# Kernel tuning notes

Measured on AMD Instinct MI355X. Metric: run time of the kernel, lower is better.

The kernel has to match this reference:

```python
import jax, jax.numpy as jnp
import numpy as np

B, L, D, H, R = 2, 128, 256, 8, 4
DK = D // H  # 32
EPS = 1e-6


def setup_inputs() -> dict:
    key = jax.random.key(0)
    ks = jax.random.split(key, 12)
    q = jax.random.normal(ks[0], (B, L, D), jnp.float32)
    k = jax.random.normal(ks[1], (B, L, D), jnp.float32)
    v = jax.random.normal(ks[2], (B, L, D), jnp.float32)
    t = jnp.sort(jax.random.uniform(ks[3], (B, L), jnp.float32), axis=-1)
    omega = jax.random.uniform(ks[4], (B, L, L), jnp.float32)
    mask = jnp.triu(jnp.ones((L, L), bool), 1)  # True = masked (causal)
    xav = (2.0 / (D + D)) ** 0.5
    Wq = jax.random.normal(ks[5], (D, H * DK), jnp.float32) * xav
    Wk = jax.random.normal(ks[6], (D, H * DK), jnp.float32) * xav
    Wv = jax.random.normal(ks[7], (D, H * DK), jnp.float32) * xav
    s = jax.random.uniform(ks[8], (R,), jnp.float32) + 0.1  # ODE time-decay scales
    fc_w = jax.random.normal(ks[9], (H * DK, D), jnp.float32) * xav
    fc_b = jnp.zeros((D,), jnp.float32)
    ln_g = jnp.ones((D,), jnp.float32)
    ln_b = jnp.zeros((D,), jnp.float32)
    return {"q": q, "k": k, "v": v, "t": t, "omega": omega, "mask": mask,
            "Wq": Wq, "Wk": Wk, "Wv": Wv, "s": s,
            "fc_w": fc_w, "fc_b": fc_b, "ln_g": ln_g, "ln_b": ln_b}


def _ode_proj(x, W, phi):
    # x: (B,L,D), W: (D,H*DK), phi: (B,L,L,R) time kernel
    p = x @ W                                       # (B,L,H*DK)
    y = p[:, None, :, None, :] * phi[..., None]     # (B,L,L,R,H*DK)
    y = y.reshape(B, L, L, R, H, DK)
    return y.transpose(0, 4, 1, 2, 3, 5)            # (B,H,L,L,R,DK)


def reference(q, k, v, t, omega, mask, Wq, Wk, Wv, s, fc_w, fc_b, ln_g, ln_b):
    temp = DK ** 0.5
    residual = q
    # pre-LayerNorm on q (normalize_before=True)
    mu = q.mean(-1, keepdims=True)
    var = q.var(-1, keepdims=True)
    qn = (q - mu) / jnp.sqrt(var + EPS) * ln_g + ln_b
    # continuous-time kernel phi[b,i,j,r] = exp(-|t_i - t_j| * s_r)
    dt = jnp.abs(t[:, :, None] - t[:, None, :])     # (B,L,L)
    phi = jnp.exp(-dt[..., None] * s)               # (B,L,L,R)
    q6 = _ode_proj(qn, Wq, phi)                     # (B,H,L,L,R,DK)
    k6 = _ode_proj(k, Wk, phi)
    v6 = _ode_proj(v, Wv, phi)
    # attn = (q/temp * k * omega).sum(-1).sum(-1)
    attn = jnp.einsum('bhijrd,bhijrd,bij->bhij', q6 / temp, k6, omega)
    attn = jnp.where(mask[None, None, :, :], -1e9, attn)
    attn = jax.nn.softmax(attn, axis=-1)            # (B,H,L,L)
    vsum = v6.sum(axis=4)                           # sum over R -> (B,H,L,L,DK)
    out = jnp.einsum('bhij,bhijd->bhid', attn, vsum)  # (B,H,L,DK)
    out = out.transpose(0, 2, 1, 3).reshape(B, L, H * DK)
    out = out @ fc_w + fc_b + residual              # dropout = identity (eval)
    return (out, attn)
```

## Files before the change

kernel.cpp:

```cpp
#include <hip/hip_runtime.h>

#define B_  2
#define L_  128
#define D_  256
#define H_  8
#define R_  4
#define DK_ 32
#define BL_ (B_*L_)
#define SXP 260
#define SQH 132
#define SWP 129

__device__ __forceinline__ float wredsum64(float v) {
    #pragma unroll
    for (int m = 32; m >= 1; m >>= 1) v += __shfl_xor(v, m, 64);
    return v;
}
__device__ __forceinline__ float wredmax64(float v) {
    #pragma unroll
    for (int m = 32; m >= 1; m >>= 1) v = fmaxf(v, __shfl_xor(v, m, 64));
    return v;
}

__global__ __launch_bounds__(256) void k_proj(
    const float* __restrict__ q, const float* __restrict__ k, const float* __restrict__ v,
    const float* __restrict__ Wq, const float* __restrict__ Wk, const float* __restrict__ Wv,
    const float* __restrict__ ln_g, const float* __restrict__ ln_b,
    float* __restrict__ pv, float* __restrict__ qkpart)
{
    const int blk = blockIdx.x;
    const int rowTile = blk >> 4;
    const int cg = blk & 15;
    const int rbase = rowTile * 4;
    const int tid = threadIdx.x;

    __shared__ __align__(16) float sx[3][4 * SXP];
    __shared__ __align__(16) float partF[16 * 4 * 16];
    __shared__ float spq[4][16], spk[4][16];

    {
        const int r = tid >> 6, f4c = tid & 63;
        #pragma unroll
        for (int p = 0; p < 3; ++p) {
            const float* src = (p == 0 ? q : (p == 1 ? k : v)) + (size_t)(rbase + r) * D_;
            *reinterpret_cast<float4*>(&sx[p][r * SXP + f4c * 4]) =
                reinterpret_cast<const float4*>(src)[f4c];
        }
    }
    __syncthreads();

    {
        const int r = tid >> 6, lane = tid & 63;
        float x0 = sx[0][r * SXP + lane];
        float x1 = sx[0][r * SXP + lane + 64];
        float x2 = sx[0][r * SXP + lane + 128];
        float x3 = sx[0][r * SXP + lane + 192];
        float s1 = x0 + x1 + x2 + x3;
        float s2 = x0*x0 + x1*x1 + x2*x2 + x3*x3;
        #pragma unroll
        for (int m = 32; m >= 1; m >>= 1) {
            s1 += __shfl_xor(s1, m, 64);
            s2 += __shfl_xor(s2, m, 64);
        }
        const float mu = s1 * (1.0f / D_);
        const float rs = rsqrtf(s2 * (1.0f / D_) - mu * mu + 1e-6f);
        sx[0][r * SXP + lane      ] = (x0 - mu) * rs * ln_g[lane      ] + ln_b[lane      ];
        sx[0][r * SXP + lane +  64] = (x1 - mu) * rs * ln_g[lane +  64] + ln_b[lane +  64];
        sx[0][r * SXP + lane + 128] = (x2 - mu) * rs * ln_g[lane + 128] + ln_b[lane + 128];
        sx[0][r * SXP + lane + 192] = (x3 - mu) * rs * ln_g[lane + 192] + ln_b[lane + 192];
    }
    __syncthreads();

    const int kg  = tid >> 4;
    const int row = (tid >> 2) & 3;
    const int c4  = tid & 3;
    const int gc4 = cg * 4 + c4;
    const int kbase = kg * 16;

    #pragma unroll
    for (int m = 0; m < 3; ++m) {
        const float4* W4 = reinterpret_cast<const float4*>(m == 0 ? Wq : (m == 1 ? Wk : Wv));
        float4 a = {0, 0, 0, 0};
        #pragma unroll
        for (int kk = 0; kk < 16; ++kk) {
            const int kr = kbase + kk;
            const float x = sx[m][row * SXP + kr];
            const float4 w = W4[kr * 64 + gc4];
            a.x += x * w.x; a.y += x * w.y; a.z += x * w.z; a.w += x * w.w;
        }
        *reinterpret_cast<float4*>(&partF[(kg * 16 + row * 4 + c4) * 4]) = a;
        __syncthreads();
        if (tid < 64) {
            const int rr = tid >> 4, cc = tid & 15;
            float sum = 0.f;
            #pragma unroll
            for (int g = 0; g < 16; ++g) sum += partF[g * 64 + rr * 16 + cc];
            if      (m == 0) spq[rr][cc] = sum;
            else if (m == 1) spk[rr][cc] = sum;
            else             pv[(size_t)(rbase + rr) * D_ + cg * 16 + cc] = sum;
        }
        __syncthreads();
    }

    if (tid < 64) {
        const int rr = tid >> 4, cc = tid & 15;
        float d = spq[rr][cc] * spk[rr][cc];
        #pragma unroll
        for (int m = 8; m >= 1; m >>= 1) d += __shfl_xor(d, m, 64);
        if (cc == 0) qkpart[(size_t)(rbase + rr) * 16 + cg] = d;
    }
}

__global__ __launch_bounds__(512) void k_attn(
    const float* __restrict__ t, const float* __restrict__ omega, const float* __restrict__ s,
    const float* __restrict__ pv, const float* __restrict__ qkpart,
    const float* __restrict__ fc_w, const float* __restrict__ fc_b,
    const float* __restrict__ q, float* __restrict__ dout)
{
    const int blk   = blockIdx.x;
    const int b     = blk >> 5;
    const int itile = blk & 31;
    const int ibase = itile * 4;
    const int tid = threadIdx.x;
    const int w = tid >> 6, lane = tid & 63;

    __shared__ __align__(16) float sQKp[L_ * 16];
    __shared__ __align__(16) float sQKh[H_ * SQH];
    __shared__ __align__(16) float sOm[4 * L_];
    __shared__ __align__(16) float sPhi[4 * L_], sPsi[4 * L_];
    __shared__ __align__(16) float sW[H_ * 4 * SWP];
    __shared__ __align__(16) float partF[8 * 4 * 64 * 4];
    __shared__ __align__(16) float sMid[4 * SXP];
    __shared__ float st[L_], sS[R_];

    {
        const float4* qkp4 = reinterpret_cast<const float4*>(qkpart + (size_t)b * L_ * 16);
        reinterpret_cast<float4*>(sQKp)[tid] = qkp4[tid];
        if (tid < 128)
            reinterpret_cast<float4*>(sOm)[tid] =
                reinterpret_cast<const float4*>(omega + ((size_t)(b * L_ + ibase)) * L_)[tid];
        if (tid < 32)
            reinterpret_cast<float4*>(st)[tid] =
                reinterpret_cast<const float4*>(t + (size_t)b * L_)[tid];
        if (tid < R_) sS[tid] = s[tid];
    }
    __syncthreads();

    {
        const int wi = tid >> 7, j = tid & 127;
        const float dtv = fabsf(st[ibase + wi] - st[j]);
        float Phi = 0.f, Psi = 0.f;
        #pragma unroll
        for (int r = 0; r < R_; ++r) {
            const float e = expf(-dtv * sS[r]);
            Phi += e;
            Psi += e * e;
        }
        sPhi[wi * L_ + j] = Phi;
        sPsi[wi * L_ + j] = Psi;
    }
    #pragma unroll
    for (int p = 0; p < 2; ++p) {
        const int idx = tid + p * 512;
        const int j = idx >> 3, h = idx & 7;
        sQKh[h * SQH + j] = sQKp[j * 16 + 2 * h] + sQKp[j * 16 + 2 * h + 1];
    }
    __syncthreads();

    {
        const int il = w >> 1;
        const int i  = ibase + il;
        const int hb = (w & 1) * 4;
        const float invtemp = 0.17677669529663687f;
        const int j0 = lane, j1 = lane + 64;
        const float c0 = sOm[il*L_ + j0] * sPsi[il*L_ + j0] * invtemp;
        const float c1 = sOm[il*L_ + j1] * sPsi[il*L_ + j1] * invtemp;
        const float ph0 = sPhi[il*L_ + j0], ph1 = sPhi[il*L_ + j1];
        #pragma unroll
        for (int hh = 0; hh < 4; ++hh) {
            const int h = hb + hh;
            float l0 = (j0 <= i) ? c0 * sQKh[h * SQH + j0] : -3.0e38f;
            float l1 = (j1 <= i) ? c1 * sQKh[h * SQH + j1] : -3.0e38f;
            const float mx = wredmax64(fmaxf(l0, l1));
            const float e0 = (j0 <= i) ? expf(l0 - mx) : 0.f;
            const float e1 = (j1 <= i) ? expf(l1 - mx) : 0.f;
            const float inv = 1.0f / wredsum64(e0 + e1);
            const float a0 = e0 * inv, a1 = e1 * inv;
            const size_t ab = (size_t)BL_ * D_ + (((size_t)(b * H_ + h) * L_ + i) * L_);
            dout[ab + j0] = a0;
            dout[ab + j1] = a1;
            sW[(h * 4 + il) * SWP + j0] = a0 * ph0;
            sW[(h * 4 + il) * SWP + j1] = a1 * ph1;
        }
    }
    __syncthreads();

    {
        const int c = lane, jg = w;
        const int h = c >> 3;
        const float4* pv4 = reinterpret_cast<const float4*>(pv + (size_t)b * L_ * D_);
        float4 acc[4];
        #pragma unroll
        for (int il = 0; il < 4; ++il) acc[il] = make_float4(0, 0, 0, 0);
        #pragma unroll
        for (int jj = 0; jj < 16; ++jj) {
            const int j = jg * 16 + jj;
            const float4 p = pv4[j * 64 + c];
            #pragma unroll
            for (int il = 0; il < 4; ++il) {
                const float wgt = sW[(h * 4 + il) * SWP + j];
                acc[il].x += wgt * p.x; acc[il].y += wgt * p.y;
                acc[il].z += wgt * p.z; acc[il].w += wgt * p.w;
            }
        }
        #pragma unroll
        for (int il = 0; il < 4; ++il)
            *reinterpret_cast<float4*>(&partF[((jg * 4 + il) * 64 + c) * 4]) = acc[il];
    }
    __syncthreads();
    if (tid < 256) {
        const int il = tid >> 6, c = tid & 63;
        float4 sum = make_float4(0, 0, 0, 0);
        #pragma unroll
        for (int g = 0; g < 8; ++g) {
            const float4 p = *reinterpret_cast<float4*>(&partF[((g * 4 + il) * 64 + c) * 4]);
            sum.x += p.x; sum.y += p.y; sum.z += p.z; sum.w += p.w;
        }
        *reinterpret_cast<float4*>(&sMid[il * SXP + c * 4]) = sum;
    }
    __syncthreads();

    {
        const int kseg = w, c4 = lane;
        const float4* fw4 = reinterpret_cast<const float4*>(fc_w);
        float4 acc[4];
        #pragma unroll
        for (int r = 0; r < 4; ++r) acc[r] = make_float4(0, 0, 0, 0);
        #pragma unroll
        for (int kk = 0; kk < 32; ++kk) {
            const int k = kseg * 32 + kk;
            const float4 wv = fw4[k * 64 + c4];
            #pragma unroll
            for (int r = 0; r < 4; ++r) {
                const float x = sMid[r * SXP + k];
                acc[r].x += x * wv.x; acc[r].y += x * wv.y;
                acc[r].z += x * wv.z; acc[r].w += x * wv.w;
            }
        }
        #pragma unroll
        for (int r = 0; r < 4; ++r)
            *reinterpret_cast<float4*>(&partF[((kseg * 4 + r) * 64 + c4) * 4]) = acc[r];
    }
    __syncthreads();
    if (tid < 256) {
        const int r = tid >> 6, c4 = tid & 63;
        const float4 bb = reinterpret_cast<const float4*>(fc_b)[c4];
        const float4 res = reinterpret_cast<const float4*>(q)[((size_t)(b * L_ + ibase + r)) * 64 + c4];
        float4 sum = make_float4(bb.x + res.x, bb.y + res.y, bb.z + res.z, bb.w + res.w);
        #pragma unroll
        for (int g = 0; g < 8; ++g) {
            const float4 p = *reinterpret_cast<float4*>(&partF[((g * 4 + r) * 64 + c4) * 4]);
            sum.x += p.x; sum.y += p.y; sum.z += p.z; sum.w += p.w;
        }
        reinterpret_cast<float4*>(dout)[((size_t)(b * L_ + ibase + r)) * 64 + c4] = sum;
    }
}

extern "C" void kernel_launch(void* const* d_in, const int* in_sizes, int n_in,
                              void* d_out, int out_size, void* d_ws, size_t ws_size,
                              hipStream_t stream) {
    const float* q     = (const float*)d_in[0];
    const float* k     = (const float*)d_in[1];
    const float* v     = (const float*)d_in[2];
    const float* t     = (const float*)d_in[3];
    const float* omega = (const float*)d_in[4];
    const float* Wq    = (const float*)d_in[6];
    const float* Wk    = (const float*)d_in[7];
    const float* Wv    = (const float*)d_in[8];
    const float* s     = (const float*)d_in[9];
    const float* fc_w  = (const float*)d_in[10];
    const float* fc_b  = (const float*)d_in[11];
    const float* ln_g  = (const float*)d_in[12];
    const float* ln_b  = (const float*)d_in[13];

    float* ws     = (float*)d_ws;
    float* pv     = ws;
    float* qkpart = ws + 65536;
    float* out    = (float*)d_out;

    hipLaunchKernelGGL(k_proj, dim3(1024), dim3(256), 0, stream,
                       q, k, v, Wq, Wk, Wv, ln_g, ln_b, pv, qkpart);
    hipLaunchKernelGGL(k_attn, dim3(64), dim3(512), 0, stream,
                       t, omega, s, pv, qkpart, fc_w, fc_b, q, out);
}
```

Baseline: 96.67 us.

## Fuse projection and attention into one cooperative kernel with grid sync

Merges the projection kernel and the attention kernel into a single cooperative launch of 256 blocks of 512 threads, separated by a grid-wide barrier, with shared memory reused through a union. The projection stage is retiled so each block computes 64 output columns for 4 rows and does the Q, K and V products in one fused loop. The goal is to remove the second launch and the inter-kernel gap. In exchange it adds grid-sync overhead, leaves most blocks idle after the barrier, and each block now holds the larger shared-memory footprint.

```diff
diff --git a/kernel.cpp b/kernel.cpp
--- a/kernel.cpp
+++ b/kernel.cpp
@@ -1,4 +1,5 @@
 #include <hip/hip_runtime.h>
+#include <hip/hip_cooperative_groups.h>
 
 #define B_  2
 #define L_  128
@@ -11,6 +12,8 @@
 #define SQH 132
 #define SWP 129
 
+namespace cg = cooperative_groups;
+
 __device__ __forceinline__ float wredsum64(float v) {
     #pragma unroll
     for (int m = 32; m >= 1; m >>= 1) v += __shfl_xor(v, m, 64);
@@ -22,148 +25,159 @@
     return v;
 }
 
-__global__ __launch_bounds__(256) void k_proj(
+struct __align__(16) SMemA {
+    float sx[3][4 * SXP];
+    float partF[3][2048];
+};
+struct __align__(16) SMemB {
+    float sQKp[2048];
+    float sQKh[H_ * SQH];
+    float sOm[4 * L_];
+    float sPhi[4 * L_];
+    float sPsi[4 * L_];
+    float sW[H_ * 4 * SWP];
+    float partF[8192];
+    float sMid[4 * SXP];
+    float st[L_];
+    float sS[R_];
+};
+union __align__(16) SMem { SMemA a; SMemB b; };
+
+__global__ __launch_bounds__(512) void k_fused(
     const float* __restrict__ q, const float* __restrict__ k, const float* __restrict__ v,
     const float* __restrict__ Wq, const float* __restrict__ Wk, const float* __restrict__ Wv,
     const float* __restrict__ ln_g, const float* __restrict__ ln_b,
-    float* __restrict__ pv, float* __restrict__ qkpart)
+    const float* __restrict__ t, const float* __restrict__ omega, const float* __restrict__ s,
+    const float* __restrict__ fc_w, const float* __restrict__ fc_b,
+    float* __restrict__ pv, float* __restrict__ qkpart, float* __restrict__ dout)
 {
+    __shared__ SMem sm;
     const int blk = blockIdx.x;
-    const int rowTile = blk >> 4;
-    const int cg = blk & 15;
-    const int rbase = rowTile * 4;
     const int tid = threadIdx.x;
 
-    __shared__ __align__(16) float sx[3][4 * SXP];
-    __shared__ __align__(16) float partF[16 * 4 * 16];
-    __shared__ float spq[4][16], spk[4][16];
-
-    {
-        const int r = tid >> 6, f4c = tid & 63;
-        #pragma unroll
-        for (int p = 0; p < 3; ++p) {
+    {
+        const int rowTile = blk >> 2;
+        const int cgA     = blk & 3;
+        const int rbase   = rowTile * 4;
+
+        for (int i = tid; i < 768; i += 512) {
+            const int p = i >> 8, r = (i >> 6) & 3, f4c = i & 63;
             const float* src = (p == 0 ? q : (p == 1 ? k : v)) + (size_t)(rbase + r) * D_;
-            *reinterpret_cast<float4*>(&sx[p][r * SXP + f4c * 4]) =
+            *reinterpret_cast<float4*>(&sm.a.sx[p][r * SXP + f4c * 4]) =
                 reinterpret_cast<const float4*>(src)[f4c];
         }
-    }
-    __syncthreads();
-
-    {
-        const int r = tid >> 6, lane = tid & 63;
-        float x0 = sx[0][r * SXP + lane];
-        float x1 = sx[0][r * SXP + lane + 64];
-        float x2 = sx[0][r * SXP + lane + 128];
-        float x3 = sx[0][r * SXP + lane + 192];
-        float s1 = x0 + x1 + x2 + x3;
-        float s2 = x0*x0 + x1*x1 + x2*x2 + x3*x3;
-        #pragma unroll
-        for (int m = 32; m >= 1; m >>= 1) {
-            s1 += __shfl_xor(s1, m, 64);
-            s2 += __shfl_xor(s2, m, 64);
-        }
-        const float mu = s1 * (1.0f / D_);
-        const float rs = rsqrtf(s2 * (1.0f / D_) - mu * mu + 1e-6f);
-        sx[0][r * SXP + lane      ] = (x0 - mu) * rs * ln_g[lane      ] + ln_b[lane      ];
-        sx[0][r * SXP + lane +  64] = (x1 - mu) * rs * ln_g[lane +  64] + ln_b[lane +  64];
-        sx[0][r * SXP + lane + 128] = (x2 - mu) * rs * ln_g[lane + 128] + ln_b[lane + 128];
-        sx[0][r * SXP + lane + 192] = (x3 - mu) * rs * ln_g[lane + 192] + ln_b[lane + 192];
-    }
-    __syncthreads();
-
-    const int kg  = tid >> 4;
-    const int row = (tid >> 2) & 3;
-    const int c4  = tid & 3;
-    const int gc4 = cg * 4 + c4;
-    const int kbase = kg * 16;
-
-    #pragma unroll
-    for (int m = 0; m < 3; ++m) {
-        const float4* W4 = reinterpret_cast<const float4*>(m == 0 ? Wq : (m == 1 ? Wk : Wv));
-        float4 a = {0, 0, 0, 0};
-        #pragma unroll
-        for (int kk = 0; kk < 16; ++kk) {
+        __syncthreads();
+
+        if (tid < 256) {
+            const int r = tid >> 6, lane = tid & 63;
+            float x0 = sm.a.sx[0][r * SXP + lane];
+            float x1 = sm.a.sx[0][r * SXP + lane + 64];
+            float x2 = sm.a.sx[0][r * SXP + lane + 128];
+            float x3 = sm.a.sx[0][r * SXP + lane + 192];
+            float s1 = x0 + x1 + x2 + x3;
+            float s2 = x0*x0 + x1*x1 + x2*x2 + x3*x3;
+            #pragma unroll
+            for (int m = 32; m >= 1; m >>= 1) {
+                s1 += __shfl_xor(s1, m, 64);
+                s2 += __shfl_xor(s2, m, 64);
+            }
+            const float mu = s1 * (1.0f / D_);
+            const float rs = rsqrtf(s2 * (1.0f / D_) - mu * mu + 1e-6f);
+            sm.a.sx[0][r * SXP + lane      ] = (x0 - mu) * rs * ln_g[lane      ] + ln_b[lane      ];
+            sm.a.sx[0][r * SXP + lane +  64] = (x1 - mu) * rs * ln_g[lane +  64] + ln_b[lane +  64];
+            sm.a.sx[0][r * SXP + lane + 128] = (x2 - mu) * rs * ln_g[lane + 128] + ln_b[lane + 128];
+            sm.a.sx[0][r * SXP + lane + 192] = (x3 - mu) * rs * ln_g[lane + 192] + ln_b[lane + 192];
+        }
+        __syncthreads();
+
+        const int kg  = tid >> 6;
+        const int row = (tid >> 4) & 3;
+        const int c4  = tid & 15;
+        const int gc4 = cgA * 16 + c4;
+        const int kbase = kg * 32;
+        const float4* Wq4 = reinterpret_cast<const float4*>(Wq);
+        const float4* Wk4 = reinterpret_cast<const float4*>(Wk);
+        const float4* Wv4 = reinterpret_cast<const float4*>(Wv);
+        float4 aq = {0,0,0,0}, ak = {0,0,0,0}, av = {0,0,0,0};
+        #pragma unroll 8
+        for (int kk = 0; kk < 32; ++kk) {
             const int kr = kbase + kk;
-            const float x = sx[m][row * SXP + kr];
-            const float4 w = W4[kr * 64 + gc4];
-            a.x += x * w.x; a.y += x * w.y; a.z += x * w.z; a.w += x * w.w;
-        }
-        *reinterpret_cast<float4*>(&partF[(kg * 16 + row * 4 + c4) * 4]) = a;
+            const float xq = sm.a.sx[0][row * SXP + kr];
+            const float xk = sm.a.sx[1][row * SXP + kr];
+            const float xv = sm.a.sx[2][row * SXP + kr];
+            const float4 wq = Wq4[kr * 64 + gc4];
+            const float4 wk = Wk4[kr * 64 + gc4];
+            const float4 wv = Wv4[kr * 64 + gc4];
+            aq.x += xq * wq.x; aq.y += xq * wq.y; aq.z += xq * wq.z; aq.w += xq * wq.w;
+            ak.x += xk * wk.x; ak.y += xk * wk.y; ak.z += xk * wk.z; ak.w += xk * wk.w;
+            av.x += xv * wv.x; av.y += xv * wv.y; av.z += xv * wv.z; av.w += xv * wv.w;
+        }
+        const int pidx = (kg * 64 + row * 16 + c4) * 4;
+        *reinterpret_cast<float4*>(&sm.a.partF[0][pidx]) = aq;
+        *reinterpret_cast<float4*>(&sm.a.partF[1][pidx]) = ak;
+        *reinterpret_cast<float4*>(&sm.a.partF[2][pidx]) = av;
         __syncthreads();
-        if (tid < 64) {
-            const int rr = tid >> 4, cc = tid & 15;
-            float sum = 0.f;
-            #pragma unroll
-            for (int g = 0; g < 16; ++g) sum += partF[g * 64 + rr * 16 + cc];
-            if      (m == 0) spq[rr][cc] = sum;
-            else if (m == 1) spk[rr][cc] = sum;
-            else             pv[(size_t)(rbase + rr) * D_ + cg * 16 + cc] = sum;
-        }
-        __syncthreads();
-    }
-
-    if (tid < 64) {
-        const int rr = tid >> 4, cc = tid & 15;
-        float d = spq[rr][cc] * spk[rr][cc];
-        #pragma unroll
-        for (int m = 8; m >= 1; m >>= 1) d += __shfl_xor(d, m, 64);
-        if (cc == 0) qkpart[(size_t)(rbase + rr) * 16 + cg] = d;
-    }
-}
-
-__global__ __launch_bounds__(512) void k_attn(
-    const float* __restrict__ t, const float* __restrict__ omega, const float* __restrict__ s,
-    const float* __restrict__ pv, const float* __restrict__ qkpart,
-    const float* __restrict__ fc_w, const float* __restrict__ fc_b,
-    const float* __restrict__ q, float* __restrict__ dout)
-{
-    const int blk   = blockIdx.x;
+
+        if (tid < 256) {
+            const int rr = tid >> 6, cf = tid & 63;
+            float sq = 0.f, sk = 0.f, sv = 0.f;
+            #pragma unroll
+            for (int g = 0; g < 8; ++g) {
+                const int idx = g * 256 + rr * 64 + cf;
+                sq += sm.a.partF[0][idx];
+                sk += sm.a.partF[1][idx];
+                sv += sm.a.partF[2][idx];
+            }
+            pv[(size_t)(rbase + rr) * D_ + cgA * 64 + cf] = sv;
+            float d = sq * sk;
+            #pragma unroll
+            for (int m = 8; m >= 1; m >>= 1) d += __shfl_xor(d, m, 64);
+            if ((cf & 15) == 0)
+                qkpart[(size_t)(rbase + rr) * 16 + cgA * 4 + (cf >> 4)] = d;
+        }
+    }
+
+    __threadfence();
+    cg::this_grid().sync();
+
+    if (blk >= 64) return;
+
     const int b     = blk >> 5;
     const int itile = blk & 31;
     const int ibase = itile * 4;
-    const int tid = threadIdx.x;
     const int w = tid >> 6, lane = tid & 63;
 
-    __shared__ __align__(16) float sQKp[L_ * 16];
-    __shared__ __align__(16) float sQKh[H_ * SQH];
-    __shared__ __align__(16) float sOm[4 * L_];
-    __shared__ __align__(16) float sPhi[4 * L_], sPsi[4 * L_];
-    __shared__ __align__(16) float sW[H_ * 4 * SWP];
-    __shared__ __align__(16) float partF[8 * 4 * 64 * 4];
-    __shared__ __align__(16) float sMid[4 * SXP];
-    __shared__ float st[L_], sS[R_];
-
     {
         const float4* qkp4 = reinterpret_cast<const float4*>(qkpart + (size_t)b * L_ * 16);
-        reinterpret_cast<float4*>(sQKp)[tid] = qkp4[tid];
+        reinterpret_cast<float4*>(sm.b.sQKp)[tid] = qkp4[tid];
         if (tid < 128)
-            reinterpret_cast<float4*>(sOm)[tid] =
+            reinterpret_cast<float4*>(sm.b.sOm)[tid] =
                 reinterpret_cast<const float4*>(omega + ((size_t)(b * L_ + ibase)) * L_)[tid];
         if (tid < 32)
-            reinterpret_cast<float4*>(st)[tid] =
+            reinterpret_cast<float4*>(sm.b.st)[tid] =
                 reinterpret_cast<const float4*>(t + (size_t)b * L_)[tid];
-        if (tid < R_) sS[tid] = s[tid];
+        if (tid < R_) sm.b.sS[tid] = s[tid];
     }
     __syncthreads();
 
     {
         const int wi = tid >> 7, j = tid & 127;
-        const float dtv = fabsf(st[ibase + wi] - st[j]);
+        const float dtv = fabsf(sm.b.st[ibase + wi] - sm.b.st[j]);
         float Phi = 0.f, Psi = 0.f;
         #pragma unroll
         for (int r = 0; r < R_; ++r) {
-            const float e = expf(-dtv * sS[r]);
+            const float e = expf(-dtv * sm.b.sS[r]);
             Phi += e;
             Psi += e * e;
         }
-        sPhi[wi * L_ + j] = Phi;
-        sPsi[wi * L_ + j] = Psi;
+        sm.b.sPhi[wi * L_ + j] = Phi;
+        sm.b.sPsi[wi * L_ + j] = Psi;
     }
     #pragma unroll
     for (int p = 0; p < 2; ++p) {
         const int idx = tid + p * 512;
         const int j = idx >> 3, h = idx & 7;
-        sQKh[h * SQH + j] = sQKp[j * 16 + 2 * h] + sQKp[j * 16 + 2 * h + 1];
+        sm.b.sQKh[h * SQH + j] = sm.b.sQKp[j * 16 + 2 * h] + sm.b.sQKp[j * 16 + 2 * h + 1];
     }
     __syncthreads();
 
@@ -173,14 +187,14 @@
         const int hb = (w & 1) * 4;
         const float invtemp = 0.17677669529663687f;
         const int j0 = lane, j1 = lane + 64;
-        const float c0 = sOm[il*L_ + j0] * sPsi[il*L_ + j0] * invtemp;
-        const float c1 = sOm[il*L_ + j1] * sPsi[il*L_ + j1] * invtemp;
-        const float ph0 = sPhi[il*L_ + j0], ph1 = sPhi[il*L_ + j1];
+        const float c0 = sm.b.sOm[il*L_ + j0] * sm.b.sPsi[il*L_ + j0] * invtemp;
+        const float c1 = sm.b.sOm[il*L_ + j1] * sm.b.sPsi[il*L_ + j1] * invtemp;
+        const float ph0 = sm.b.sPhi[il*L_ + j0], ph1 = sm.b.sPhi[il*L_ + j1];
         #pragma unroll
         for (int hh = 0; hh < 4; ++hh) {
             const int h = hb + hh;
-            float l0 = (j0 <= i) ? c0 * sQKh[h * SQH + j0] : -3.0e38f;
-            float l1 = (j1 <= i) ? c1 * sQKh[h * SQH + j1] : -3.0e38f;
+            float l0 = (j0 <= i) ? c0 * sm.b.sQKh[h * SQH + j0] : -3.0e38f;
+            float l1 = (j1 <= i) ? c1 * sm.b.sQKh[h * SQH + j1] : -3.0e38f;
             const float mx = wredmax64(fmaxf(l0, l1));
             const float e0 = (j0 <= i) ? expf(l0 - mx) : 0.f;
             const float e1 = (j1 <= i) ? expf(l1 - mx) : 0.f;
@@ -189,8 +203,8 @@
             const size_t ab = (size_t)BL_ * D_ + (((size_t)(b * H_ + h) * L_ + i) * L_);
             dout[ab + j0] = a0;
             dout[ab + j1] = a1;
-            sW[(h * 4 + il) * SWP + j0] = a0 * ph0;
-            sW[(h * 4 + il) * SWP + j1] = a1 * ph1;
+            sm.b.sW[(h * 4 + il) * SWP + j0] = a0 * ph0;
+            sm.b.sW[(h * 4 + il) * SWP + j1] = a1 * ph1;
         }
     }
     __syncthreads();
@@ -208,14 +222,14 @@
             const float4 p = pv4[j * 64 + c];
             #pragma unroll
             for (int il = 0; il < 4; ++il) {
-                const float wgt = sW[(h * 4 + il) * SWP + j];
+                const float wgt = sm.b.sW[(h * 4 + il) * SWP + j];
                 acc[il].x += wgt * p.x; acc[il].y += wgt * p.y;
                 acc[il].z += wgt * p.z; acc[il].w += wgt * p.w;
             }
         }
         #pragma unroll
         for (int il = 0; il < 4; ++il)
-            *reinterpret_cast<float4*>(&partF[((jg * 4 + il) * 64 + c) * 4]) = acc[il];
+            *reinterpret_cast<float4*>(&sm.b.partF[((jg * 4 + il) * 64 + c) * 4]) = acc[il];
     }
     __syncthreads();
     if (tid < 256) {
@@ -223,10 +237,10 @@
         float4 sum = make_float4(0, 0, 0, 0);
         #pragma unroll
         for (int g = 0; g < 8; ++g) {
-            const float4 p = *reinterpret_cast<float4*>(&partF[((g * 4 + il) * 64 + c) * 4]);
+            const float4 p = *reinterpret_cast<float4*>(&sm.b.partF[((g * 4 + il) * 64 + c) * 4]);
             sum.x += p.x; sum.y += p.y; sum.z += p.z; sum.w += p.w;
         }
-        *reinterpret_cast<float4*>(&sMid[il * SXP + c * 4]) = sum;
+        *reinterpret_cast<float4*>(&sm.b.sMid[il * SXP + c * 4]) = sum;
     }
     __syncthreads();
 
@@ -238,18 +252,18 @@
         for (int r = 0; r < 4; ++r) acc[r] = make_float4(0, 0, 0, 0);
         #pragma unroll
         for (int kk = 0; kk < 32; ++kk) {
-            const int k = kseg * 32 + kk;
-            const float4 wv = fw4[k * 64 + c4];
+            const int kx = kseg * 32 + kk;
+            const float4 wv = fw4[kx * 64 + c4];
             #pragma unroll
             for (int r = 0; r < 4; ++r) {
-                const float x = sMid[r * SXP + k];
+                const float x = sm.b.sMid[r * SXP + kx];
                 acc[r].x += x * wv.x; acc[r].y += x * wv.y;
                 acc[r].z += x * wv.z; acc[r].w += x * wv.w;
             }
         }
         #pragma unroll
         for (int r = 0; r < 4; ++r)
-            *reinterpret_cast<float4*>(&partF[((kseg * 4 + r) * 64 + c4) * 4]) = acc[r];
+            *reinterpret_cast<float4*>(&sm.b.partF[((kseg * 4 + r) * 64 + c4) * 4]) = acc[r];
     }
     __syncthreads();
     if (tid < 256) {
@@ -259,7 +273,7 @@
         float4 sum = make_float4(bb.x + res.x, bb.y + res.y, bb.z + res.z, bb.w + res.w);
         #pragma unroll
         for (int g = 0; g < 8; ++g) {
-            const float4 p = *reinterpret_cast<float4*>(&partF[((g * 4 + r) * 64 + c4) * 4]);
+            const float4 p = *reinterpret_cast<float4*>(&sm.b.partF[((g * 4 + r) * 64 + c4) * 4]);
             sum.x += p.x; sum.y += p.y; sum.z += p.z; sum.w += p.w;
         }
         reinterpret_cast<float4*>(dout)[((size_t)(b * L_ + ibase + r)) * 64 + c4] = sum;
@@ -288,8 +302,13 @@
     float* qkpart = ws + 65536;
     float* out    = (float*)d_out;
 
-    hipLaunchKernelGGL(k_proj, dim3(1024), dim3(256), 0, stream,
-                       q, k, v, Wq, Wk, Wv, ln_g, ln_b, pv, qkpart);
-    hipLaunchKernelGGL(k_attn, dim3(64), dim3(512), 0, stream,
-                       t, omega, s, pv, qkpart, fc_w, fc_b, q, out);
+    void* args[] = {
+        (void*)&q, (void*)&k, (void*)&v,
+        (void*)&Wq, (void*)&Wk, (void*)&Wv,
+        (void*)&ln_g, (void*)&ln_b,
+        (void*)&t, (void*)&omega, (void*)&s,
+        (void*)&fc_w, (void*)&fc_b,
+        (void*)&pv, (void*)&qkpart, (void*)&out
+    };
+    hipLaunchCooperativeKernel((void*)k_fused, dim3(256), dim3(512), args, 0, stream);
 }
```

Measured after the change: 187.3 us. +93.8%, slower.

## Restructure projection to fuse Q/K/V GEMVs and halve attention row tile

Applied to the files above, without the earlier changes.

The projection kernel now computes Q, K and V partial products together in one loop, with 512 threads covering 64 output columns per block. This cuts the block count from 1024 to 256, removes the per-matrix sync and reduce rounds, and makes each block re-read its staged inputs less often. The attention kernel now processes 2 query rows per block instead of 4, doubling the grid to 128 blocks so more compute units are busy. The cost is that fc_w and pv are re-read from global memory by twice as many attention blocks.

```diff
diff --git a/kernel.cpp b/kernel.cpp
--- a/kernel.cpp
+++ b/kernel.cpp
@@ -22,34 +22,30 @@
     return v;
 }
 
-__global__ __launch_bounds__(256) void k_proj(
+__global__ __launch_bounds__(512) void k_proj(
     const float* __restrict__ q, const float* __restrict__ k, const float* __restrict__ v,
     const float* __restrict__ Wq, const float* __restrict__ Wk, const float* __restrict__ Wv,
     const float* __restrict__ ln_g, const float* __restrict__ ln_b,
     float* __restrict__ pv, float* __restrict__ qkpart)
 {
     const int blk = blockIdx.x;
-    const int rowTile = blk >> 4;
-    const int cg = blk & 15;
-    const int rbase = rowTile * 4;
+    const int rowTile = blk >> 2;
+    const int cgA     = blk & 3;
+    const int rbase   = rowTile * 4;
     const int tid = threadIdx.x;
 
     __shared__ __align__(16) float sx[3][4 * SXP];
-    __shared__ __align__(16) float partF[16 * 4 * 16];
-    __shared__ float spq[4][16], spk[4][16];
-
-    {
-        const int r = tid >> 6, f4c = tid & 63;
-        #pragma unroll
-        for (int p = 0; p < 3; ++p) {
-            const float* src = (p == 0 ? q : (p == 1 ? k : v)) + (size_t)(rbase + r) * D_;
-            *reinterpret_cast<float4*>(&sx[p][r * SXP + f4c * 4]) =
-                reinterpret_cast<const float4*>(src)[f4c];
-        }
-    }
-    __syncthreads();
-
-    {
+    __shared__ __align__(16) float partF[3][2048];
+
+    for (int i = tid; i < 768; i += 512) {
+        const int p = i >> 8, r = (i >> 6) & 3, f4c = i & 63;
+        const float* src = (p == 0 ? q : (p == 1 ? k : v)) + (size_t)(rbase + r) * D_;
+        *reinterpret_cast<float4*>(&sx[p][r * SXP + f4c * 4]) =
+            reinterpret_cast<const float4*>(src)[f4c];
+    }
+    __syncthreads();
+
+    if (tid < 256) {
         const int r = tid >> 6, lane = tid & 63;
         float x0 = sx[0][r * SXP + lane];
         float x1 = sx[0][r * SXP + lane + 64];
@@ -71,43 +67,50 @@
     }
     __syncthreads();
 
-    const int kg  = tid >> 4;
-    const int row = (tid >> 2) & 3;
-    const int c4  = tid & 3;
-    const int gc4 = cg * 4 + c4;
-    const int kbase = kg * 16;
-
-    #pragma unroll
-    for (int m = 0; m < 3; ++m) {
-        const float4* W4 = reinterpret_cast<const float4*>(m == 0 ? Wq : (m == 1 ? Wk : Wv));
-        float4 a = {0, 0, 0, 0};
-        #pragma unroll
-        for (int kk = 0; kk < 16; ++kk) {
-            const int kr = kbase + kk;
-            const float x = sx[m][row * SXP + kr];
-            const float4 w = W4[kr * 64 + gc4];
-            a.x += x * w.x; a.y += x * w.y; a.z += x * w.z; a.w += x * w.w;
-        }
-        *reinterpret_cast<float4*>(&partF[(kg * 16 + row * 4 + c4) * 4]) = a;
-        __syncthreads();
-        if (tid < 64) {
-            const int rr = tid >> 4, cc = tid & 15;
-            float sum = 0.f;
-            #pragma unroll
-            for (int g = 0; g < 16; ++g) sum += partF[g * 64 + rr * 16 + cc];
-            if      (m == 0) spq[rr][cc] = sum;
-            else if (m == 1) spk[rr][cc] = sum;
-            else             pv[(size_t)(rbase + rr) * D_ + cg * 16 + cc] = sum;
-        }
-        __syncthreads();
-    }
-
-    if (tid < 64) {
-        const int rr = tid >> 4, cc = tid & 15;
-        float d = spq[rr][cc] * spk[rr][cc];
+    const int kg  = tid >> 6;
+    const int row = (tid >> 4) & 3;
+    const int c4  = tid & 15;
+    const int gc4 = cgA * 16 + c4;
+    const int kbase = kg * 32;
+    const float4* Wq4 = reinterpret_cast<const float4*>(Wq);
+    const float4* Wk4 = reinterpret_cast<const float4*>(Wk);
+    const float4* Wv4 = reinterpret_cast<const float4*>(Wv);
+    float4 aq = {0,0,0,0}, ak = {0,0,0,0}, av = {0,0,0,0};
+    #pragma unroll 8
+    for (int kk = 0; kk < 32; ++kk) {
+        const int kr = kbase + kk;
+        const float xq = sx[0][row * SXP + kr];
+        const float xk = sx[1][row * SXP + kr];
+        const float xv = sx[2][row * SXP + kr];
+        const float4 wq = Wq4[kr * 64 + gc4];
+        const float4 wk = Wk4[kr * 64 + gc4];
+        const float4 wv = Wv4[kr * 64 + gc4];
+        aq.x += xq * wq.x; aq.y += xq * wq.y; aq.z += xq * wq.z; aq.w += xq * wq.w;
+        ak.x += xk * wk.x; ak.y += xk * wk.y; ak.z += xk * wk.z; ak.w += xk * wk.w;
+        av.x += xv * wv.x; av.y += xv * wv.y; av.z += xv * wv.z; av.w += xv * wv.w;
+    }
+    const int pidx = (kg * 64 + row * 16 + c4) * 4;
+    *reinterpret_cast<float4*>(&partF[0][pidx]) = aq;
+    *reinterpret_cast<float4*>(&partF[1][pidx]) = ak;
+    *reinterpret_cast<float4*>(&partF[2][pidx]) = av;
+    __syncthreads();
+
+    if (tid < 256) {
+        const int rr = tid >> 6, cf = tid & 63;
+        float sq = 0.f, sk = 0.f, sv = 0.f;
+        #pragma unroll
+        for (int g = 0; g < 8; ++g) {
+            const int idx = g * 256 + rr * 64 + cf;
+            sq += partF[0][idx];
+            sk += partF[1][idx];
+            sv += partF[2][idx];
+        }
+        pv[(size_t)(rbase + rr) * D_ + cgA * 64 + cf] = sv;
+        float d = sq * sk;
         #pragma unroll
         for (int m = 8; m >= 1; m >>= 1) d += __shfl_xor(d, m, 64);
-        if (cc == 0) qkpart[(size_t)(rbase + rr) * 16 + cg] = d;
+        if ((cf & 15) == 0)
+            qkpart[(size_t)(rbase + rr) * 16 + cgA * 4 + (cf >> 4)] = d;
     }
 }
 
@@ -118,25 +121,25 @@
     const float* __restrict__ q, float* __restrict__ dout)
 {
     const int blk   = blockIdx.x;
-    const int b     = blk >> 5;
-    const int itile = blk & 31;
-    const int ibase = itile * 4;
+    const int b     = blk >> 6;
+    const int itile = blk & 63;
+    const int ibase = itile * 2;
     const int tid = threadIdx.x;
     const int w = tid >> 6, lane = tid & 63;
 
     __shared__ __align__(16) float sQKp[L_ * 16];
     __shared__ __align__(16) float sQKh[H_ * SQH];
-    __shared__ __align__(16) float sOm[4 * L_];
-    __shared__ __align__(16) float sPhi[4 * L_], sPsi[4 * L_];
-    __shared__ __align__(16) float sW[H_ * 4 * SWP];
-    __shared__ __align__(16) float partF[8 * 4 * 64 * 4];
-    __shared__ __align__(16) float sMid[4 * SXP];
+    __shared__ __align__(16) float sOm[2 * L_];
+    __shared__ __align__(16) float sPhi[2 * L_], sPsi[2 * L_];
+    __shared__ __align__(16) float sW[H_ * 2 * SWP];
+    __shared__ __align__(16) float partF[8 * 2 * 64 * 4];
+    __shared__ __align__(16) float sMid[2 * SXP];
     __shared__ float st[L_], sS[R_];
 
     {
         const float4* qkp4 = reinterpret_cast<const float4*>(qkpart + (size_t)b * L_ * 16);
         reinterpret_cast<float4*>(sQKp)[tid] = qkp4[tid];
-        if (tid < 128)
+        if (tid < 64)
             reinterpret_cast<float4*>(sOm)[tid] =
                 reinterpret_cast<const float4*>(omega + ((size_t)(b * L_ + ibase)) * L_)[tid];
         if (tid < 32)
@@ -146,7 +149,7 @@
     }
     __syncthreads();
 
-    {
+    if (tid < 256) {
         const int wi = tid >> 7, j = tid & 127;
         const float dtv = fabsf(st[ibase + wi] - st[j]);
         float Phi = 0.f, Psi = 0.f;
@@ -168,16 +171,16 @@
     __syncthreads();
 
     {
-        const int il = w >> 1;
+        const int il = w >> 2;
         const int i  = ibase + il;
-        const int hb = (w & 1) * 4;
+        const int hb = (w & 3) * 2;
         const float invtemp = 0.17677669529663687f;
         const int j0 = lane, j1 = lane + 64;
         const float c0 = sOm[il*L_ + j0] * sPsi[il*L_ + j0] * invtemp;
         const float c1 = sOm[il*L_ + j1] * sPsi[il*L_ + j1] * invtemp;
         const float ph0 = sPhi[il*L_ + j0], ph1 = sPhi[il*L_ + j1];
         #pragma unroll
-        for (int hh = 0; hh < 4; ++hh) {
+        for (int hh = 0; hh < 2; ++hh) {
             const int h = hb + hh;
             float l0 = (j0 <= i) ? c0 * sQKh[h * SQH + j0] : -3.0e38f;
             float l1 = (j1 <= i) ? c1 * sQKh[h * SQH + j1] : -3.0e38f;
@@ -189,8 +192,8 @@
             const size_t ab = (size_t)BL_ * D_ + (((size_t)(b * H_ + h) * L_ + i) * L_);
             dout[ab + j0] = a0;
             dout[ab + j1] = a1;
-            sW[(h * 4 + il) * SWP + j0] = a0 * ph0;
-            sW[(h * 4 + il) * SWP + j1] = a1 * ph1;
+            sW[(h * 2 + il) * SWP + j0] = a0 * ph0;
+            sW[(h * 2 + il) * SWP + j1] = a1 * ph1;
         }
     }
     __syncthreads();
@@ -199,31 +202,31 @@
         const int c = lane, jg = w;
         const int h = c >> 3;
         const float4* pv4 = reinterpret_cast<const float4*>(pv + (size_t)b * L_ * D_);
-        float4 acc[4];
-        #pragma unroll
-        for (int il = 0; il < 4; ++il) acc[il] = make_float4(0, 0, 0, 0);
+        float4 acc[2];
+        #pragma unroll
+        for (int il = 0; il < 2; ++il) acc[il] = make_float4(0, 0, 0, 0);
         #pragma unroll
         for (int jj = 0; jj < 16; ++jj) {
             const int j = jg * 16 + jj;
             const float4 p = pv4[j * 64 + c];
             #pragma unroll
-            for (int il = 0; il < 4; ++il) {
-                const float wgt = sW[(h * 4 + il) * SWP + j];
+            for (int il = 0; il < 2; ++il) {
+                const float wgt = sW[(h * 2 + il) * SWP + j];
                 acc[il].x += wgt * p.x; acc[il].y += wgt * p.y;
                 acc[il].z += wgt * p.z; acc[il].w += wgt * p.w;
             }
         }
         #pragma unroll
-        for (int il = 0; il < 4; ++il)
-            *reinterpret_cast<float4*>(&partF[((jg * 4 + il) * 64 + c) * 4]) = acc[il];
-    }
-    __syncthreads();
-    if (tid < 256) {
+        for (int il = 0; il < 2; ++il)
+            *reinterpret_cast<float4*>(&partF[((jg * 2 + il) * 64 + c) * 4]) = acc[il];
+    }
+    __syncthreads();
+    if (tid < 128) {
         const int il = tid >> 6, c = tid & 63;
         float4 sum = make_float4(0, 0, 0, 0);
         #pragma unroll
         for (int g = 0; g < 8; ++g) {
-            const float4 p = *reinterpret_cast<float4*>(&partF[((g * 4 + il) * 64 + c) * 4]);
+            const float4 p = *reinterpret_cast<float4*>(&partF[((g * 2 + il) * 64 + c) * 4]);
             sum.x += p.x; sum.y += p.y; sum.z += p.z; sum.w += p.w;
         }
         *reinterpret_cast<float4*>(&sMid[il * SXP + c * 4]) = sum;
@@ -233,33 +236,33 @@
     {
         const int kseg = w, c4 = lane;
         const float4* fw4 = reinterpret_cast<const float4*>(fc_w);
-        float4 acc[4];
-        #pragma unroll
-        for (int r = 0; r < 4; ++r) acc[r] = make_float4(0, 0, 0, 0);
+        float4 acc[2];
+        #pragma unroll
+        for (int r = 0; r < 2; ++r) acc[r] = make_float4(0, 0, 0, 0);
         #pragma unroll
         for (int kk = 0; kk < 32; ++kk) {
-            const int k = kseg * 32 + kk;
-            const float4 wv = fw4[k * 64 + c4];
+            const int kx = kseg * 32 + kk;
+            const float4 wv = fw4[kx * 64 + c4];
             #pragma unroll
-            for (int r = 0; r < 4; ++r) {
-                const float x = sMid[r * SXP + k];
+            for (int r = 0; r < 2; ++r) {
+                const float x = sMid[r * SXP + kx];
                 acc[r].x += x * wv.x; acc[r].y += x * wv.y;
                 acc[r].z += x * wv.z; acc[r].w += x * wv.w;
             }
         }
         #pragma unroll
-        for (int r = 0; r < 4; ++r)
-            *reinterpret_cast<float4*>(&partF[((kseg * 4 + r) * 64 + c4) * 4]) = acc[r];
-    }
-    __syncthreads();
-    if (tid < 256) {
+        for (int r = 0; r < 2; ++r)
+            *reinterpret_cast<float4*>(&partF[((kseg * 2 + r) * 64 + c4) * 4]) = acc[r];
+    }
+    __syncthreads();
+    if (tid < 128) {
         const int r = tid >> 6, c4 = tid & 63;
         const float4 bb = reinterpret_cast<const float4*>(fc_b)[c4];
         const float4 res = reinterpret_cast<const float4*>(q)[((size_t)(b * L_ + ibase + r)) * 64 + c4];
         float4 sum = make_float4(bb.x + res.x, bb.y + res.y, bb.z + res.z, bb.w + res.w);
         #pragma unroll
         for (int g = 0; g < 8; ++g) {
-            const float4 p = *reinterpret_cast<float4*>(&partF[((g * 4 + r) * 64 + c4) * 4]);
+            const float4 p = *reinterpret_cast<float4*>(&partF[((g * 2 + r) * 64 + c4) * 4]);
             sum.x += p.x; sum.y += p.y; sum.z += p.z; sum.w += p.w;
         }
         reinterpret_cast<float4*>(dout)[((size_t)(b * L_ + ibase + r)) * 64 + c4] = sum;
@@ -288,8 +291,8 @@
     float* qkpart = ws + 65536;
     float* out    = (float*)d_out;
 
-    hipLaunchKernelGGL(k_proj, dim3(1024), dim3(256), 0, stream,
+    hipLaunchKernelGGL(k_proj, dim3(256), dim3(512), 0, stream,
                        q, k, v, Wq, Wk, Wv, ln_g, ln_b, pv, qkpart);
-    hipLaunchKernelGGL(k_attn, dim3(64), dim3(512), 0, stream,
+    hipLaunchKernelGGL(k_attn, dim3(128), dim3(512), 0, stream,
                        t, omega, s, pv, qkpart, fc_w, fc_b, q, out);
 }
```

New measurement: 113.0 us. 16.9% more time.
